# Performance work log

Measured on AMD Instinct MI355X. Metric: run time of the kernel, lower is better.

## Reference

```python
import jax, jax.numpy as jnp
import numpy as np

NUM_HEADS = 16


def setup_inputs() -> dict:
    key = jax.random.key(0)
    ks = jax.random.split(key, 5)
    B, N, D = 2, 2048, 1024
    scale = 1.0 / np.sqrt(D)  # roughly xavier-ish magnitude for weights
    return {
        "x": jax.random.normal(ks[0], (B, N, D), dtype=jnp.float32),
        "W_query": jax.random.normal(ks[1], (D, D), dtype=jnp.float32) * scale,
        "W_key": jax.random.normal(ks[2], (D, D), dtype=jnp.float32) * scale,
        "W_value": jax.random.normal(ks[3], (D, D), dtype=jnp.float32) * scale,
        "W_output": jax.random.normal(ks[4], (D, D), dtype=jnp.float32) * scale,
    }


def reference(x, W_query, W_key, W_value, W_output):
    # x: [B, N, D]; weights: [D, D]
    B, N, D = x.shape
    H = NUM_HEADS
    hd = D // H

    def mh_embed(W):
        # linear_embedding then split heads: [B, N, D] -> [B, H, N, hd]
        y = jnp.einsum("bnd,de->bne", x, W)
        return y.reshape(B, N, H, hd).transpose(0, 2, 1, 3)

    q = mh_embed(W_query)
    k = mh_embed(W_key)
    v = mh_embed(W_value)

    # NOTE: source scales by token_dim**-0.5 (full model dim), not head_dim
    attn = jnp.einsum("bhnd,bhmd->bhnm", q, k) * (D ** -0.5)
    attn = jax.nn.softmax(attn, axis=-1)
    out = jnp.einsum("bhnm,bhmd->bhnd", attn, v)  # [B, H, N, hd]

    out = out.transpose(0, 2, 1, 3).reshape(B, N, D)  # merge heads
    out = jnp.einsum("bnd,de->bne", out, W_output)
    return out
```

## Files before the change

kernel.cpp:

```cpp
#include <hip/hip_runtime.h>

#define D_MODEL 1024
#define N_TOK   2048
#define NHEAD   16
#define HDIM    64
#define BATCH   2
#define M_TOT   (BATCH*N_TOK)

typedef unsigned short u16;
typedef __bf16 bf16x8 __attribute__((ext_vector_type(8)));
typedef float  f32x4  __attribute__((ext_vector_type(4)));

#define QSCALE 0.04508422002777439f

__device__ __forceinline__ u16 f2bf(float f) {
  union { float f; unsigned u; } v; v.f = f;
  unsigned r = v.u + 0x7fffu + ((v.u >> 16) & 1u);
  return (u16)(r >> 16);
}

__device__ __forceinline__ unsigned pk2bf(float a, float b) {
#if __has_builtin(__builtin_amdgcn_cvt_pk_bf16_f32)
  typedef __bf16 bf16x2_t __attribute__((ext_vector_type(2)));
  bf16x2_t r = __builtin_amdgcn_cvt_pk_bf16_f32(a, b);
  union { bf16x2_t v; unsigned u; } c; c.v = r; return c.u;
#else
  return (unsigned)f2bf(a) | ((unsigned)f2bf(b) << 16);
#endif
}

__device__ __forceinline__ void gl2lds16(const void* g, void* l) {
  __builtin_amdgcn_global_load_lds(
      (__attribute__((address_space(1))) void*)g,
      (__attribute__((address_space(3))) void*)l, 16, 0, 0);
}

__global__ void cast_kernel(const float* __restrict__ src, u16* __restrict__ dst, int n4) {
  int i = blockIdx.x * blockDim.x + threadIdx.x;
  int stride = gridDim.x * blockDim.x;
  for (; i < n4; i += stride) {
    float4 v = ((const float4*)src)[i];
    ushort4 o;
    o.x = f2bf(v.x); o.y = f2bf(v.y); o.z = f2bf(v.z); o.w = f2bf(v.w);
    ((ushort4*)dst)[i] = o;
  }
}

__global__ void transpose_cast4(const float* __restrict__ s0, const float* __restrict__ s1,
                                const float* __restrict__ s2, const float* __restrict__ s3,
                                u16* __restrict__ d0, u16* __restrict__ d1,
                                u16* __restrict__ d2, u16* __restrict__ d3) {
  const float* src; u16* dst;
  switch (blockIdx.z) {
    case 0:  src = s0; dst = d0; break;
    case 1:  src = s1; dst = d1; break;
    case 2:  src = s2; dst = d2; break;
    default: src = s3; dst = d3; break;
  }
  float sc = (blockIdx.z == 0) ? QSCALE : 1.0f;
  __shared__ float tile[32][33];
  int x = blockIdx.x * 32 + threadIdx.x;
  int ybase = blockIdx.y * 32;
#pragma unroll
  for (int r = 0; r < 4; ++r)
    tile[threadIdx.y + r*8][threadIdx.x] = src[(size_t)(ybase + threadIdx.y + r*8)*D_MODEL + x];
  __syncthreads();
#pragma unroll
  for (int r = 0; r < 4; ++r)
    dst[(size_t)(blockIdx.x*32 + threadIdx.y + r*8)*D_MODEL + ybase + threadIdx.x] =
        f2bf(tile[threadIdx.x][threadIdx.y + r*8] * sc);
}

__device__ __forceinline__ void gemm_body(const u16* __restrict__ A,
                                          const u16* __restrict__ Bt,
                                          void* __restrict__ Cout, int mode) {
  __shared__ __attribute__((aligned(16))) u16 lA[128*32];
  __shared__ __attribute__((aligned(16))) u16 lB[128*32];
  const int t = threadIdx.x;
  const int lane = t & 63, w = t >> 6;
  const int wm = w >> 1, wn = w & 1;
  const int q4 = lane >> 4, l15 = lane & 15;
  const int m0 = blockIdx.y * 128, n0 = blockIdx.x * 128;

  f32x4 acc[4][4] = {};

  for (int k0 = 0; k0 < D_MODEL; k0 += 32) {
    __syncthreads();
#pragma unroll
    for (int i = 0; i < 2; ++i) {
      int c = i*256 + t;
      int row = c >> 2;
      int clog = (c & 3) ^ (row & 3);
      gl2lds16(A  + (size_t)(m0 + row)*D_MODEL + k0 + clog*8, lA + c*8);
      gl2lds16(Bt + (size_t)(n0 + row)*D_MODEL + k0 + clog*8, lB + c*8);
    }
    __syncthreads();
    bf16x8 af[4], bfr[4];
#pragma unroll
    for (int mi = 0; mi < 4; ++mi) {
      int r = wm*64 + mi*16 + l15;
      af[mi] = *(const bf16x8*)(lA + r*32 + ((q4 ^ (r & 3)) * 8));
    }
#pragma unroll
    for (int ni = 0; ni < 4; ++ni) {
      int r = wn*64 + ni*16 + l15;
      bfr[ni] = *(const bf16x8*)(lB + r*32 + ((q4 ^ (r & 3)) * 8));
    }
#pragma unroll
    for (int mi = 0; mi < 4; ++mi)
#pragma unroll
      for (int ni = 0; ni < 4; ++ni)
        acc[mi][ni] = __builtin_amdgcn_mfma_f32_16x16x32_bf16(af[mi], bfr[ni], acc[mi][ni], 0, 0, 0);
  }

#pragma unroll
  for (int mi = 0; mi < 4; ++mi) {
#pragma unroll
    for (int ni = 0; ni < 4; ++ni) {
      const int tok0 = m0 + wm*64 + mi*16 + q4*4;
      const int col  = n0 + wn*64 + ni*16 + l15;
      if (mode == 0) {
        u16* D = (u16*)Cout;
#pragma unroll
        for (int r = 0; r < 4; ++r) {
          int tok = tok0 + r;
          int b = tok >> 11, n = tok & (N_TOK-1);
          int h = col >> 6, d = col & (HDIM-1);
          D[(((size_t)(b*NHEAD + h))*N_TOK + n)*HDIM + d] = f2bf(acc[mi][ni][r]);
        }
      } else if (mode == 2) {
        int b = tok0 >> 11, n = tok0 & (N_TOK-1);
        int h = col >> 6, d = col & (HDIM-1);
        ushort4 pk;
        pk.x = f2bf(acc[mi][ni][0]); pk.y = f2bf(acc[mi][ni][1]);
        pk.z = f2bf(acc[mi][ni][2]); pk.w = f2bf(acc[mi][ni][3]);
        *(ushort4*)((u16*)Cout + ((size_t)(b*NHEAD + h)*HDIM + d)*N_TOK + n) = pk;
      } else {
        float* D = (float*)Cout;
#pragma unroll
        for (int r = 0; r < 4; ++r)
          D[(size_t)(tok0 + r)*D_MODEL + col] = acc[mi][ni][r];
      }
    }
  }
}

__global__ __launch_bounds__(256) void qkv_kernel(const u16* __restrict__ xb,
    const u16* __restrict__ wqt, const u16* __restrict__ wkt, const u16* __restrict__ wvt,
    u16* __restrict__ Q, u16* __restrict__ K, u16* __restrict__ Vt) {
  int z = blockIdx.z;
  const u16* B = (z == 0) ? wqt : (z == 1) ? wkt : wvt;
  void* C = (z == 0) ? (void*)Q : (z == 1) ? (void*)K : (void*)Vt;
  gemm_body(xb, B, C, (z == 2) ? 2 : 0);
}

__global__ __launch_bounds__(256) void out_kernel(const u16* __restrict__ ctx,
    const u16* __restrict__ wot, float* __restrict__ out) {
  gemm_body(ctx, wot, (void*)out, 3);
}

__global__ __launch_bounds__(256, 3) void attn_kernel(const u16* __restrict__ Qg,
    const u16* __restrict__ Kg, const u16* __restrict__ Vtg, u16* __restrict__ ctx) {
  __shared__ __attribute__((aligned(16))) u16 lds[24576];
  u16* lKP = lds;
  u16* lV  = lds + 16384;
  const int t = threadIdx.x;
  const int lane = t & 63, w = t >> 6;
  const int q4 = lane >> 4, l15 = lane & 15;
  const int bh = blockIdx.y;
  const int qw0 = blockIdx.x * 128 + w * 32;
  const size_t kvBase = (size_t)bh * (N_TOK * HDIM);
  u16* myP = lds + w * 4096;

  bf16x8 qf[2][2];
#pragma unroll
  for (int ni = 0; ni < 2; ++ni)
#pragma unroll
    for (int kk = 0; kk < 2; ++kk)
      qf[ni][kk] = *(const bf16x8*)(Qg + kvBase +
                    (size_t)(qw0 + ni*16 + l15)*HDIM + kk*32 + q4*8);

  f32x4 accO[4][2] = {};
  float lsum[2] = {0.f, 0.f};

  for (int kv0 = 0; kv0 < N_TOK; kv0 += 128) {
    __syncthreads();
#pragma unroll
    for (int i = 0; i < 4; ++i) {
      int c = i*256 + t;
      { int r = c >> 3, ch = c & 7;
        gl2lds16(Kg + kvBase + (size_t)(kv0 + r)*HDIM + ((ch ^ (r & 7)) * 8),
                 lKP + c*8); }
      { int d = c >> 4, cv = c & 15;
        gl2lds16(Vtg + kvBase + (size_t)d*N_TOK + kv0 + ((cv ^ (d & 7)) * 8),
                 lV + c*8); }
    }
    __syncthreads();

    f32x4 accS[8][2] = {};
#pragma unroll
    for (int kk = 0; kk < 2; ++kk)
#pragma unroll
      for (int mi = 0; mi < 8; ++mi) {
        int kv = mi*16 + l15;
        bf16x8 a = *(const bf16x8*)(lKP + kv*64 + (((kk*4 + q4) ^ (kv & 7)) * 8));
#pragma unroll
        for (int ni = 0; ni < 2; ++ni)
          accS[mi][ni] = __builtin_amdgcn_mfma_f32_16x16x32_bf16(a, qf[ni][kk], accS[mi][ni], 0, 0, 0);
      }

    __syncthreads();

#pragma unroll
    for (int mi = 0; mi < 8; ++mi)
#pragma unroll
      for (int ni = 0; ni < 2; ++ni) {
        float p0 = __builtin_amdgcn_exp2f(accS[mi][ni][0]);
        float p1 = __builtin_amdgcn_exp2f(accS[mi][ni][1]);
        float p2 = __builtin_amdgcn_exp2f(accS[mi][ni][2]);
        float p3 = __builtin_amdgcn_exp2f(accS[mi][ni][3]);
        lsum[ni] += (p0 + p1) + (p2 + p3);
        uint2 u; u.x = pk2bf(p0, p1); u.y = pk2bf(p2, p3);
        int qloc = ni*16 + l15;
        int kv4 = mi*4 + q4;
        *(uint2*)(myP + qloc*128 + ((kv4 >> 1) ^ (qloc & 7))*8 + (kv4 & 1)*4) = u;
      }

#pragma unroll
    for (int kk2 = 0; kk2 < 4; ++kk2) {
      bf16x8 bp[2];
#pragma unroll
      for (int ni = 0; ni < 2; ++ni)
        bp[ni] = *(const bf16x8*)(myP + (ni*16 + l15)*128 +
                                  (((kk2*4 + q4) ^ (l15 & 7)) * 8));
#pragma unroll
      for (int mi = 0; mi < 4; ++mi) {
        int d = mi*16 + l15;
        bf16x8 av = *(const bf16x8*)(lV + d*128 + (((kk2*4 + q4) ^ (d & 7)) * 8));
#pragma unroll
        for (int ni = 0; ni < 2; ++ni)
          accO[mi][ni] = __builtin_amdgcn_mfma_f32_16x16x32_bf16(av, bp[ni], accO[mi][ni], 0, 0, 0);
      }
    }
  }

  const int b = bh >> 4, head = bh & (NHEAD-1);
#pragma unroll
  for (int ni = 0; ni < 2; ++ni) {
    float ls = lsum[ni];
    ls += __shfl_xor(ls, 16);
    ls += __shfl_xor(ls, 32);
    float inv = 1.0f / ls;
    size_t rb = ((size_t)(b*N_TOK + qw0 + ni*16 + l15))*D_MODEL + head*HDIM + q4*4;
#pragma unroll
    for (int mi = 0; mi < 4; ++mi) {
      uint2 u;
      u.x = pk2bf(accO[mi][ni][0]*inv, accO[mi][ni][1]*inv);
      u.y = pk2bf(accO[mi][ni][2]*inv, accO[mi][ni][3]*inv);
      *(uint2*)(ctx + rb + mi*16) = u;
    }
  }
}

extern "C" void kernel_launch(void* const* d_in, const int* in_sizes, int n_in,
                              void* d_out, int out_size, void* d_ws, size_t ws_size,
                              hipStream_t stream) {
  const float* x  = (const float*)d_in[0];
  const float* Wq = (const float*)d_in[1];
  const float* Wk = (const float*)d_in[2];
  const float* Wv = (const float*)d_in[3];
  const float* Wo = (const float*)d_in[4];
  float* out = (float*)d_out;

  char* ws = (char*)d_ws;
  u16* xb  = (u16*)(ws);
  u16* wqt = (u16*)(ws + (8u  << 20));
  u16* wkt = (u16*)(ws + (10u << 20));
  u16* wvt = (u16*)(ws + (12u << 20));
  u16* wot = (u16*)(ws + (14u << 20));
  u16* Qw  = (u16*)(ws + (16u << 20));
  u16* Kw  = (u16*)(ws + (24u << 20));
  u16* Vtw = (u16*)(ws + (32u << 20));
  u16* ctx = (u16*)(ws + (40u << 20));
  (void)in_sizes; (void)n_in; (void)out_size; (void)ws_size;

  cast_kernel<<<1024, 256, 0, stream>>>(x, xb, M_TOT*D_MODEL/4);
  transpose_cast4<<<dim3(32, 32, 4), dim3(32, 8), 0, stream>>>(Wq, Wk, Wv, Wo,
                                                               wqt, wkt, wvt, wot);
  qkv_kernel<<<dim3(8, 32, 3), 256, 0, stream>>>(xb, wqt, wkt, wvt, Qw, Kw, Vtw);
  attn_kernel<<<dim3(16, 32), 256, 0, stream>>>(Qw, Kw, Vtw, ctx);
  out_kernel<<<dim3(8, 32), 256, 0, stream>>>(ctx, wot, out);
}
```

Baseline: 234.6 us.

## Split attention KV range across two blocks and add combine kernel; fuse prep casts

Attention now splits each query tile's KV sequence into two halves handled by separate blocks (doubling the grid from 512 to 1024 blocks), writing fp32 partial outputs and row sums that a new combine kernel sums and normalizes into bf16 context. The inner loop is restructured to compute S, exponentiate and do PV in half-tiles, which shrinks the P buffer and removes one barrier per iteration. The x cast and the weight transpose-casts are merged into a single prep launch. The trade is better CU occupancy and less per-block serial work against extra fp32 partial traffic (about 32 MB written and read) and one more kernel launch.

```diff
diff --git a/kernel.cpp b/kernel.cpp
--- a/kernel.cpp
+++ b/kernel.cpp
@@ -35,21 +35,25 @@
       (__attribute__((address_space(3))) void*)l, 16, 0, 0);
 }
 
-__global__ void cast_kernel(const float* __restrict__ src, u16* __restrict__ dst, int n4) {
-  int i = blockIdx.x * blockDim.x + threadIdx.x;
-  int stride = gridDim.x * blockDim.x;
-  for (; i < n4; i += stride) {
-    float4 v = ((const float4*)src)[i];
-    ushort4 o;
-    o.x = f2bf(v.x); o.y = f2bf(v.y); o.z = f2bf(v.z); o.w = f2bf(v.w);
-    ((ushort4*)dst)[i] = o;
-  }
-}
-
-__global__ void transpose_cast4(const float* __restrict__ s0, const float* __restrict__ s1,
-                                const float* __restrict__ s2, const float* __restrict__ s3,
-                                u16* __restrict__ d0, u16* __restrict__ d1,
-                                u16* __restrict__ d2, u16* __restrict__ d3) {
+__global__ void prep_kernel(const float* __restrict__ x,
+                            const float* __restrict__ s0, const float* __restrict__ s1,
+                            const float* __restrict__ s2, const float* __restrict__ s3,
+                            u16* __restrict__ xb,
+                            u16* __restrict__ d0, u16* __restrict__ d1,
+                            u16* __restrict__ d2, u16* __restrict__ d3) {
+  const int t = threadIdx.y * 32 + threadIdx.x;
+  if (blockIdx.z == 4) {
+    int base = (blockIdx.y * 32 + blockIdx.x) * 256 + t;
+#pragma unroll
+    for (int r = 0; r < 4; ++r) {
+      int i = base + r * 262144;
+      float4 v = ((const float4*)x)[i];
+      ushort4 o;
+      o.x = f2bf(v.x); o.y = f2bf(v.y); o.z = f2bf(v.z); o.w = f2bf(v.w);
+      ((ushort4*)xb)[i] = o;
+    }
+    return;
+  }
   const float* src; u16* dst;
   switch (blockIdx.z) {
     case 0:  src = s0; dst = d0; break;
@@ -59,11 +63,11 @@
   }
   float sc = (blockIdx.z == 0) ? QSCALE : 1.0f;
   __shared__ float tile[32][33];
-  int x = blockIdx.x * 32 + threadIdx.x;
+  int xg = blockIdx.x * 32 + threadIdx.x;
   int ybase = blockIdx.y * 32;
 #pragma unroll
   for (int r = 0; r < 4; ++r)
-    tile[threadIdx.y + r*8][threadIdx.x] = src[(size_t)(ybase + threadIdx.y + r*8)*D_MODEL + x];
+    tile[threadIdx.y + r*8][threadIdx.x] = src[(size_t)(ybase + threadIdx.y + r*8)*D_MODEL + xg];
   __syncthreads();
 #pragma unroll
   for (int r = 0; r < 4; ++r)
@@ -160,17 +164,20 @@
 }
 
 __global__ __launch_bounds__(256, 3) void attn_kernel(const u16* __restrict__ Qg,
-    const u16* __restrict__ Kg, const u16* __restrict__ Vtg, u16* __restrict__ ctx) {
+    const u16* __restrict__ Kg, const u16* __restrict__ Vtg,
+    float* __restrict__ Opart, float* __restrict__ Lpart) {
   __shared__ __attribute__((aligned(16))) u16 lds[24576];
-  u16* lKP = lds;
-  u16* lV  = lds + 16384;
+  u16* lK = lds;
+  u16* lV = lds + 8192;
+  u16* lP = lds + 16384;
   const int t = threadIdx.x;
   const int lane = t & 63, w = t >> 6;
   const int q4 = lane >> 4, l15 = lane & 15;
   const int bh = blockIdx.y;
-  const int qw0 = blockIdx.x * 128 + w * 32;
+  const int qb = blockIdx.x >> 1, half = blockIdx.x & 1;
+  const int qw0 = qb * 128 + w * 32;
   const size_t kvBase = (size_t)bh * (N_TOK * HDIM);
-  u16* myP = lds + w * 4096;
+  u16* myP = lP + w * 2048;
 
   bf16x8 qf[2][2];
 #pragma unroll
@@ -183,83 +190,106 @@
   f32x4 accO[4][2] = {};
   float lsum[2] = {0.f, 0.f};
 
-  for (int kv0 = 0; kv0 < N_TOK; kv0 += 128) {
+  for (int it = 0; it < 8; ++it) {
+    const int kv0 = half * 1024 + it * 128;
     __syncthreads();
 #pragma unroll
     for (int i = 0; i < 4; ++i) {
       int c = i*256 + t;
       { int r = c >> 3, ch = c & 7;
         gl2lds16(Kg + kvBase + (size_t)(kv0 + r)*HDIM + ((ch ^ (r & 7)) * 8),
-                 lKP + c*8); }
+                 lK + c*8); }
       { int d = c >> 4, cv = c & 15;
-        gl2lds16(Vtg + kvBase + (size_t)d*N_TOK + kv0 + ((cv ^ (d & 7)) * 8),
+        gl2lds16(Vtg + kvBase + (size_t)d*N_TOK + kv0 + ((cv ^ (d & 15)) * 8),
                  lV + c*8); }
     }
     __syncthreads();
 
-    f32x4 accS[8][2] = {};
-#pragma unroll
-    for (int kk = 0; kk < 2; ++kk)
-#pragma unroll
-      for (int mi = 0; mi < 8; ++mi) {
-        int kv = mi*16 + l15;
-        bf16x8 a = *(const bf16x8*)(lKP + kv*64 + (((kk*4 + q4) ^ (kv & 7)) * 8));
+#pragma unroll
+    for (int h = 0; h < 2; ++h) {
+#pragma unroll
+      for (int mip = 0; mip < 4; ++mip) {
+        const int mi = h*4 + mip;
+        const int kv = mi*16 + l15;
+        f32x4 s[2] = {};
+#pragma unroll
+        for (int kk = 0; kk < 2; ++kk) {
+          bf16x8 a = *(const bf16x8*)(lK + kv*64 + (((kk*4 + q4) ^ (l15 & 7)) * 8));
+#pragma unroll
+          for (int ni = 0; ni < 2; ++ni)
+            s[ni] = __builtin_amdgcn_mfma_f32_16x16x32_bf16(a, qf[ni][kk], s[ni], 0, 0, 0);
+        }
+#pragma unroll
+        for (int ni = 0; ni < 2; ++ni) {
+          float p0 = __builtin_amdgcn_exp2f(s[ni][0]);
+          float p1 = __builtin_amdgcn_exp2f(s[ni][1]);
+          float p2 = __builtin_amdgcn_exp2f(s[ni][2]);
+          float p3 = __builtin_amdgcn_exp2f(s[ni][3]);
+          lsum[ni] += (p0 + p1) + (p2 + p3);
+          uint2 u; u.x = pk2bf(p0, p1); u.y = pk2bf(p2, p3);
+          const int qloc = ni*16 + l15;
+          const int kv8 = mip*4 + q4;
+          *(uint2*)(myP + qloc*64 + (((kv8 >> 1) ^ (qloc & 7)) * 8) + (kv8 & 1)*4) = u;
+        }
+      }
+#pragma unroll
+      for (int kk2p = 0; kk2p < 2; ++kk2p) {
+        bf16x8 bp[2];
 #pragma unroll
         for (int ni = 0; ni < 2; ++ni)
-          accS[mi][ni] = __builtin_amdgcn_mfma_f32_16x16x32_bf16(a, qf[ni][kk], accS[mi][ni], 0, 0, 0);
+          bp[ni] = *(const bf16x8*)(myP + (ni*16 + l15)*64 +
+                                    (((kk2p*4 + q4) ^ (l15 & 7)) * 8));
+#pragma unroll
+        for (int mi2 = 0; mi2 < 4; ++mi2) {
+          const int d = mi2*16 + l15;
+          const int g = (h*2 + kk2p)*4 + q4;
+          bf16x8 av = *(const bf16x8*)(lV + d*128 + ((g ^ (d & 15)) * 8));
+#pragma unroll
+          for (int ni = 0; ni < 2; ++ni)
+            accO[mi2][ni] = __builtin_amdgcn_mfma_f32_16x16x32_bf16(av, bp[ni], accO[mi2][ni], 0, 0, 0);
+        }
       }
-
-    __syncthreads();
-
-#pragma unroll
-    for (int mi = 0; mi < 8; ++mi)
-#pragma unroll
-      for (int ni = 0; ni < 2; ++ni) {
-        float p0 = __builtin_amdgcn_exp2f(accS[mi][ni][0]);
-        float p1 = __builtin_amdgcn_exp2f(accS[mi][ni][1]);
-        float p2 = __builtin_amdgcn_exp2f(accS[mi][ni][2]);
-        float p3 = __builtin_amdgcn_exp2f(accS[mi][ni][3]);
-        lsum[ni] += (p0 + p1) + (p2 + p3);
-        uint2 u; u.x = pk2bf(p0, p1); u.y = pk2bf(p2, p3);
-        int qloc = ni*16 + l15;
-        int kv4 = mi*4 + q4;
-        *(uint2*)(myP + qloc*128 + ((kv4 >> 1) ^ (qloc & 7))*8 + (kv4 & 1)*4) = u;
-      }
-
-#pragma unroll
-    for (int kk2 = 0; kk2 < 4; ++kk2) {
-      bf16x8 bp[2];
-#pragma unroll
-      for (int ni = 0; ni < 2; ++ni)
-        bp[ni] = *(const bf16x8*)(myP + (ni*16 + l15)*128 +
-                                  (((kk2*4 + q4) ^ (l15 & 7)) * 8));
-#pragma unroll
-      for (int mi = 0; mi < 4; ++mi) {
-        int d = mi*16 + l15;
-        bf16x8 av = *(const bf16x8*)(lV + d*128 + (((kk2*4 + q4) ^ (d & 7)) * 8));
-#pragma unroll
-        for (int ni = 0; ni < 2; ++ni)
-          accO[mi][ni] = __builtin_amdgcn_mfma_f32_16x16x32_bf16(av, bp[ni], accO[mi][ni], 0, 0, 0);
-      }
     }
   }
 
   const int b = bh >> 4, head = bh & (NHEAD-1);
+  float* Obase = Opart + (size_t)half * (M_TOT * D_MODEL);
 #pragma unroll
   for (int ni = 0; ni < 2; ++ni) {
     float ls = lsum[ni];
     ls += __shfl_xor(ls, 16);
     ls += __shfl_xor(ls, 32);
-    float inv = 1.0f / ls;
-    size_t rb = ((size_t)(b*N_TOK + qw0 + ni*16 + l15))*D_MODEL + head*HDIM + q4*4;
-#pragma unroll
-    for (int mi = 0; mi < 4; ++mi) {
-      uint2 u;
-      u.x = pk2bf(accO[mi][ni][0]*inv, accO[mi][ni][1]*inv);
-      u.y = pk2bf(accO[mi][ni][2]*inv, accO[mi][ni][3]*inv);
-      *(uint2*)(ctx + rb + mi*16) = u;
-    }
-  }
+    const int q = qw0 + ni*16 + l15;
+    if (q4 == 0)
+      Lpart[(size_t)half*(32*N_TOK) + bh*N_TOK + q] = ls;
+    const size_t rb = ((size_t)(b*N_TOK + q))*D_MODEL + head*HDIM + q4*4;
+#pragma unroll
+    for (int mi2 = 0; mi2 < 4; ++mi2) {
+      float4 v;
+      v.x = accO[mi2][ni][0]; v.y = accO[mi2][ni][1];
+      v.z = accO[mi2][ni][2]; v.w = accO[mi2][ni][3];
+      *(float4*)(Obase + rb + mi2*16) = v;
+    }
+  }
+}
+
+__global__ __launch_bounds__(256) void combine_kernel(const float* __restrict__ Opart,
+    const float* __restrict__ Lpart, u16* __restrict__ ctx) {
+  int i = blockIdx.x * 256 + threadIdx.x;
+  int tok = i >> 8, d4 = i & 255;
+  int n = tok & (N_TOK-1), b = tok >> 11;
+  int h = d4 >> 4;
+  int bh = b*NHEAD + h;
+  float l = Lpart[(size_t)bh*N_TOK + n] + Lpart[(size_t)(32*N_TOK) + bh*N_TOK + n];
+  float inv = 1.0f / l;
+  float4 o0 = *(const float4*)(Opart + (size_t)tok*D_MODEL + d4*4);
+  float4 o1 = *(const float4*)(Opart + (size_t)(M_TOT*D_MODEL) + (size_t)tok*D_MODEL + d4*4);
+  ushort4 o;
+  o.x = f2bf((o0.x + o1.x) * inv);
+  o.y = f2bf((o0.y + o1.y) * inv);
+  o.z = f2bf((o0.z + o1.z) * inv);
+  o.w = f2bf((o0.w + o1.w) * inv);
+  *(ushort4*)(ctx + (size_t)tok*D_MODEL + d4*4) = o;
 }
 
 extern "C" void kernel_launch(void* const* d_in, const int* in_sizes, int n_in,
@@ -273,21 +303,23 @@
   float* out = (float*)d_out;
 
   char* ws = (char*)d_ws;
-  u16* xb  = (u16*)(ws);
-  u16* wqt = (u16*)(ws + (8u  << 20));
-  u16* wkt = (u16*)(ws + (10u << 20));
-  u16* wvt = (u16*)(ws + (12u << 20));
-  u16* wot = (u16*)(ws + (14u << 20));
-  u16* Qw  = (u16*)(ws + (16u << 20));
-  u16* Kw  = (u16*)(ws + (24u << 20));
-  u16* Vtw = (u16*)(ws + (32u << 20));
-  u16* ctx = (u16*)(ws + (40u << 20));
+  u16* xb   = (u16*)(ws);
+  u16* wqt  = (u16*)(ws + (8u  << 20));
+  u16* wkt  = (u16*)(ws + (10u << 20));
+  u16* wvt  = (u16*)(ws + (12u << 20));
+  u16* wot  = (u16*)(ws + (14u << 20));
+  u16* Qw   = (u16*)(ws + (16u << 20));
+  u16* Kw   = (u16*)(ws + (24u << 20));
+  u16* Vtw  = (u16*)(ws + (32u << 20));
+  u16* ctx  = (u16*)(ws + (40u << 20));
+  float* Op = (float*)(ws + (48u << 20));
+  float* Lp = (float*)(ws + (80u << 20));
   (void)in_sizes; (void)n_in; (void)out_size; (void)ws_size;
 
-  cast_kernel<<<1024, 256, 0, stream>>>(x, xb, M_TOT*D_MODEL/4);
-  transpose_cast4<<<dim3(32, 32, 4), dim3(32, 8), 0, stream>>>(Wq, Wk, Wv, Wo,
-                                                               wqt, wkt, wvt, wot);
+  prep_kernel<<<dim3(32, 32, 5), dim3(32, 8), 0, stream>>>(x, Wq, Wk, Wv, Wo,
+                                                           xb, wqt, wkt, wvt, wot);
   qkv_kernel<<<dim3(8, 32, 3), 256, 0, stream>>>(xb, wqt, wkt, wvt, Qw, Kw, Vtw);
-  attn_kernel<<<dim3(16, 32), 256, 0, stream>>>(Qw, Kw, Vtw, ctx);
+  attn_kernel<<<dim3(32, 32), 256, 0, stream>>>(Qw, Kw, Vtw, Op, Lp);
+  combine_kernel<<<4096, 256, 0, stream>>>(Op, Lp, ctx);
   out_kernel<<<dim3(8, 32), 256, 0, stream>>>(ctx, wot, out);
 }
```

Measured after the change: 203.1 us. -13.4%, faster.
